# Kernel tuning notes

Hardware: AMD Instinct MI355X
Metric: run time of the kernel (lower is better)

Reference implementation:

```python
import jax, jax.numpy as jnp
import numpy as np

FP8_MAX = 448.0  # max finite value of float8_e4m3fn (the fwd fp8 dtype)


def fp8_quantize_dequantize(x):
    """Emulates load_ops_library.fp8_quantize followed by the dequant the
    fp8_matmul performs via its scale_inv tensors: per-tensor amax scaling,
    cast to e4m3 (round-to-nearest-even, saturating), cast back, unscale."""
    amax = jnp.max(jnp.abs(x))
    scale = FP8_MAX / jnp.maximum(amax, jnp.asarray(1e-12, x.dtype))
    q = (x * scale).astype(jnp.float8_e4m3fn).astype(x.dtype) / scale
    return q


def setup_inputs() -> dict:
    key = jax.random.key(0)
    k1, k2, k3 = jax.random.split(key, 3)
    tokens, d_in, units = 8192, 4096, 16384
    x = jax.random.normal(k1, (tokens, d_in), dtype=jnp.float32)
    # kernel ~ RandomNormal(mean=0, stddev=0.023) per the layer default
    kernel = 0.023 * jax.random.normal(k2, (d_in, units), dtype=jnp.float32)
    bias = 0.02 * jax.random.normal(k3, (units,), dtype=jnp.float32)
    return {"x": x, "kernel": kernel, "bias": bias}


def reference(x, kernel, bias):
    # fp8 path: quantize activations and kernel to e4m3, fp8 GEMM with fused
    # bias (emulated as dequantized f32 GEMM), then fused approximate gelu.
    xq = fp8_quantize_dequantize(x)          # [T, D] in e4m3 grid
    kq = fp8_quantize_dequantize(kernel)     # [D, U] in e4m3 grid
    out = jnp.dot(xq, kq) + bias             # [T, U]
    out = jax.nn.gelu(out, approximate=True) # tanh-approximate gelu
    return out
```

## Files before the change

kernel.cpp:

```cpp
#include <hip/hip_runtime.h>
#include <cstdint>
#include <cstddef>

namespace {

constexpr int T_DIM = 8192;
constexpr int D_DIM = 4096;
constexpr int U_DIM = 16384;

typedef float f32x4 __attribute__((ext_vector_type(4)));

__device__ __forceinline__ void gl_lds16(const void* g, void* l) {
  typedef const __attribute__((address_space(1))) unsigned int* gp_t;
  typedef __attribute__((address_space(3))) unsigned int* lp_t;
  __builtin_amdgcn_global_load_lds((gp_t)g, (lp_t)l, 16, 0, 0);
}

__global__ void amax_kernel(const float4* __restrict__ p, int n4,
                            unsigned* __restrict__ out) {
  float m = 0.f;
  const int stride = gridDim.x * blockDim.x;
  for (int i = blockIdx.x * blockDim.x + threadIdx.x; i < n4; i += stride) {
    float4 v = p[i];
    m = fmaxf(m, fmaxf(fmaxf(fabsf(v.x), fabsf(v.y)),
                       fmaxf(fabsf(v.z), fabsf(v.w))));
  }
#pragma unroll
  for (int off = 32; off > 0; off >>= 1)
    m = fmaxf(m, __shfl_down(m, off, 64));
  if ((threadIdx.x & 63) == 0) atomicMax(out, __float_as_uint(m));
}

__global__ void quant_x_kernel(const float4* __restrict__ x,
                               unsigned* __restrict__ xq, int n4,
                               const unsigned* __restrict__ amax_bits) {
  const float s = 448.f / fmaxf(__uint_as_float(amax_bits[0]), 1e-12f);
  const int stride = gridDim.x * blockDim.x;
  for (int i = blockIdx.x * blockDim.x + threadIdx.x; i < n4; i += stride) {
    float4 v = x[i];
    int pk = 0;
    pk = __builtin_amdgcn_cvt_pk_fp8_f32(v.x * s, v.y * s, pk, false);
    pk = __builtin_amdgcn_cvt_pk_fp8_f32(v.z * s, v.w * s, pk, true);
    xq[i] = (unsigned)pk;
  }
}

__global__ void quant_kT_kernel(const float* __restrict__ k,
                                unsigned char* __restrict__ kq,
                                const unsigned* __restrict__ amax_bits) {
  __shared__ float smf[64 * 65];
  const float s = 448.f / fmaxf(__uint_as_float(amax_bits[1]), 1e-12f);
  const int u0 = blockIdx.x * 64, d0 = blockIdx.y * 64;
  const int t = threadIdx.x;
  const int r0 = t >> 4, c4 = (t & 15) << 2;
#pragma unroll
  for (int rr = r0; rr < 64; rr += 16) {
    float4 v = *(const float4*)(k + (size_t)(d0 + rr) * U_DIM + u0 + c4);
    smf[(c4 + 0) * 65 + rr] = v.x;
    smf[(c4 + 1) * 65 + rr] = v.y;
    smf[(c4 + 2) * 65 + rr] = v.z;
    smf[(c4 + 3) * 65 + rr] = v.w;
  }
  __syncthreads();
#pragma unroll
  for (int rr = r0; rr < 64; rr += 16) {
    float a = smf[rr * 65 + c4 + 0];
    float b = smf[rr * 65 + c4 + 1];
    float c = smf[rr * 65 + c4 + 2];
    float d = smf[rr * 65 + c4 + 3];
    int pk = 0;
    pk = __builtin_amdgcn_cvt_pk_fp8_f32(a * s, b * s, pk, false);
    pk = __builtin_amdgcn_cvt_pk_fp8_f32(c * s, d * s, pk, true);
    *(unsigned*)(kq + (size_t)(u0 + rr) * D_DIM + d0 + c4) = (unsigned)pk;
  }
}


#define BAR() __builtin_amdgcn_s_barrier()
#define WLGKM() asm volatile("s_waitcnt lgkmcnt(0)" ::: "memory")
#define WVM_(N) asm volatile("s_waitcnt vmcnt(" #N ")" ::: "memory")
#define WVM(N) WVM_(N)
#define SBAR0() __builtin_amdgcn_sched_barrier(0)

#define LDA(MH)                                                         \
  do {                                                                  \
    _Pragma("unroll") for (int q2 = 0; q2 < 4; ++q2) {                  \
      _Pragma("unroll") for (int ks = 0; ks < 4; ++ks) {                \
        aR[q2][ks] = *(const long long*)&sh[aks[ks] +                   \
                                            ((MH)*64 + q2 * 16) * 128]; \
      }                                                                 \
    }                                                                   \
  } while (0)

#define LDB(NH)                                                       \
  do {                                                                \
    _Pragma("unroll") for (int j = 0; j < 2; ++j) {                   \
      _Pragma("unroll") for (int ks = 0; ks < 4; ++ks) {              \
        bR[j][ks] =                                                   \
            *(const long long*)&sh[bks[ks] + ((NH)*2 + j) * 2048];    \
      }                                                               \
    }                                                                 \
  } while (0)

#define MQ(MH, NH)                                                        \
  do {                                                                    \
    _Pragma("unroll") for (int ks = 0; ks < 4; ++ks) {                    \
      _Pragma("unroll") for (int q2 = 0; q2 < 4; ++q2) {                  \
        _Pragma("unroll") for (int j = 0; j < 2; ++j) {                   \
          acc[(MH)*4 + q2][(NH)*2 + j] =                                  \
              __builtin_amdgcn_mfma_f32_16x16x32_fp8_fp8(                 \
                  aR[q2][ks], bR[j][ks], acc[(MH)*4 + q2][(NH)*2 + j], 0, \
                  0, 0);                                                  \
        }                                                                 \
      }                                                                   \
    }                                                                     \
  } while (0)

#define STG_A(ROFF, LOFF, KB1) \
  gl_lds16(gA + (size_t)(ROFF)*D_DIM + (KB1), &sh[(LOFF) + ldst])
#define STG_B(ROFF, LOFF, KB1) \
  gl_lds16(gB + (size_t)(ROFF)*D_DIM + (KB1), &sh[65536 + (LOFF) + ldst])

#define TILE_BODY(ABUF, ANEXT, KB1, ST, VM1)                              \
  do {                                                                    \
    int aks[4], bks[4];                                                   \
    _Pragma("unroll") for (int ks = 0; ks < 4; ++ks) {                    \
      aks[ks] = ((ABUF) + arow) ^ (ks << 5);                              \
      bks[ks] = ((ABUF) + brow) ^ (ks << 5);                              \
    }                                                                     \
                              \
    LDA(0);                                                               \
    LDB(0);                                                               \
    if (ST) {                                                             \
      STG_B(0, (ANEXT) + 0, KB1);                                         \
      STG_B(128, (ANEXT) + 16384, KB1);                                   \
    }                                                                     \
    BAR();                                                                \
    WLGKM();                                                              \
    __builtin_amdgcn_s_setprio(1);                                        \
    MQ(0, 0);                                                             \
    __builtin_amdgcn_s_setprio(0);                                        \
    BAR();                                                                \
                                       \
    LDB(1);                                                               \
    if (ST) {                                                             \
      STG_B(64, (ANEXT) + 8192, KB1);                                     \
      STG_B(192, (ANEXT) + 24576, KB1);                                   \
    }                                                                     \
    BAR();                                                                \
    WLGKM();                                                              \
    __builtin_amdgcn_s_setprio(1);                                        \
    MQ(0, 1);                                                             \
    __builtin_amdgcn_s_setprio(0);                                        \
    WVM(VM1);                                                             \
    BAR();                                                                \
    SBAR0();        \
                                       \
    LDA(1);                                                               \
    LDB(0);                                                               \
    if (ST) {                                                             \
      STG_A(0, (ANEXT) + 0, KB1);                                         \
      STG_A(128, (ANEXT) + 16384, KB1);                                   \
    }                                                                     \
    BAR();                                                                \
    WLGKM();                                                              \
    __builtin_amdgcn_s_setprio(1);                                        \
    MQ(1, 0);                                                             \
    __builtin_amdgcn_s_setprio(0);                                        \
    BAR();                                                                \
                                       \
    LDB(1);                                                               \
    if (ST) {                                                             \
      STG_A(64, (ANEXT) + 8192, KB1);                                     \
      STG_A(192, (ANEXT) + 24576, KB1);                                   \
    }                                                                     \
    BAR();                                                                \
    WLGKM();                                                              \
    __builtin_amdgcn_s_setprio(1);                                        \
    MQ(1, 1);                                                             \
    __builtin_amdgcn_s_setprio(0);                                        \
    WVM(2);                                                               \
    BAR();                                                                \
    SBAR0();         \
  } while (0)

__global__ __launch_bounds__(512, 2) void gemm_fp8_kernel(
    const unsigned char* __restrict__ A, const unsigned char* __restrict__ B,
    const float* __restrict__ bias, const unsigned* __restrict__ amax_bits,
    float* __restrict__ out) {
  __shared__ __align__(128) unsigned char sh[131072];

  const int tid = threadIdx.x;
  const int lane = tid & 63;
  const int wave = tid >> 6;
  const int wr = wave >> 2, wc = wave & 3;
  const int lane15 = lane & 15;

  const int bid = (int)blockIdx.y * 64 + (int)blockIdx.x;
  const int swz = (bid & 7) * 256 + (bid >> 3);
  const size_t m0 = (size_t)(swz >> 6) * 256;
  const size_t n0 = (size_t)(swz & 63) * 256;

  const float sx = 448.f / fmaxf(__uint_as_float(amax_bits[0]), 1e-12f);
  const float sk = 448.f / fmaxf(__uint_as_float(amax_bits[1]), 1e-12f);
  const float inv_s = 1.f / (sx * sk);

  const int srow = tid >> 3;
  const int schunk = (((tid & 7) ^ (srow & 7)) << 4);
  const unsigned char* gA = A + (m0 + srow) * D_DIM + schunk;
  const unsigned char* gB = B + (n0 + srow) * D_DIM + schunk;
  const int ldst = tid * 16;

  const int kgs = (((lane >> 4) << 3) ^ ((lane & 7) << 4));
  const int arow = (wr * 128 + lane15) * 128 + kgs;
  const int brow = 65536 + (wc * 64 + lane15) * 128 + kgs;

  f32x4 acc[8][4];
#pragma unroll
  for (int i = 0; i < 8; ++i)
#pragma unroll
    for (int j = 0; j < 4; ++j) acc[i][j] = (f32x4){0.f, 0.f, 0.f, 0.f};
  long long aR[4][4];
  long long bR[2][4];

  STG_B(0, 0, 0);
  STG_B(128, 16384, 0);
  STG_B(64, 8192, 0);
  STG_B(192, 24576, 0);
  STG_A(0, 0, 0);
  STG_A(128, 16384, 0);
  STG_A(64, 8192, 0);
  STG_A(192, 24576, 0);
  asm volatile("s_waitcnt vmcnt(0)" ::: "memory");
  BAR();
  SBAR0();

  for (int tp = 0; tp < 15; ++tp) {
    const size_t kb1a = (size_t)(2 * tp + 1) * 128;
    const size_t kb1b = (size_t)(2 * tp + 2) * 128;
    TILE_BODY(0, 32768, kb1a, true, 4);
    TILE_BODY(32768, 0, kb1b, true, 4);
  }
  TILE_BODY(0, 32768, (size_t)31 * 128, true, 4);
  TILE_BODY(32768, 0, (size_t)0, false, 0);

  const int q4 = (lane >> 4) << 2;
  float bj[4];
#pragma unroll
  for (int j = 0; j < 4; ++j)
    bj[j] = bias[n0 + wc * 64 + j * 16 + lane15];

#pragma unroll
  for (int i = 0; i < 8; ++i) {
    const size_t grow_base = m0 + (size_t)(wr * 128 + i * 16 + q4);
#pragma unroll
    for (int r = 0; r < 4; ++r) {
      float* orow = out + (grow_base + r) * U_DIM + n0 + wc * 64 + lane15;
#pragma unroll
      for (int j = 0; j < 4; ++j) {
        float v = acc[i][j][r] * inv_s + bj[j];
        float uu = 0.7978845608028654f * (v + 0.044715f * v * v * v);
        float e = __expf(2.f * uu);
        float th = 1.f - 2.f / (e + 1.f);
        orow[j * 16] = 0.5f * v * (1.f + th);
      }
    }
  }
}

}

extern "C" void kernel_launch(void* const* d_in, const int* in_sizes, int n_in,
                              void* d_out, int out_size, void* d_ws,
                              size_t ws_size, hipStream_t stream) {
  const float* x = (const float*)d_in[0];
  const float* kern = (const float*)d_in[1];
  const float* bias = (const float*)d_in[2];
  float* out = (float*)d_out;

  unsigned char* ws = (unsigned char*)d_ws;
  unsigned* amax_bits = (unsigned*)ws;
  unsigned char* xq = ws + 256;
  unsigned char* kqt = ws + 256 + (size_t)T_DIM * D_DIM;

  hipMemsetAsync(d_ws, 0, 8, stream);

  amax_kernel<<<2048, 256, 0, stream>>>((const float4*)x, T_DIM * D_DIM / 4,
                                        amax_bits + 0);
  amax_kernel<<<4096, 256, 0, stream>>>((const float4*)kern, D_DIM * U_DIM / 4,
                                        amax_bits + 1);
  quant_x_kernel<<<2048, 256, 0, stream>>>((const float4*)x, (unsigned*)xq,
                                           T_DIM * D_DIM / 4, amax_bits);
  quant_kT_kernel<<<dim3(U_DIM / 64, D_DIM / 64), 256, 0, stream>>>(
      kern, kqt, amax_bits);
  gemm_fp8_kernel<<<dim3(U_DIM / 256, T_DIM / 256), 512, 0, stream>>>(
      xq, kqt, bias, amax_bits, out);
}
```

Baseline: 1.993 ms.

## Restructure GEMM tile loop into two phases with all-B register preload

Each k-tile is now split into two half-phases instead of four quarter-phases. The full B fragment set (4x4) is loaded into registers once per tile, and A fragments are loaded in small per-row-group chunks interleaved with their MFMAs. This removes several workgroup barriers and LDS waits per tile, lets LDS reads overlap with MFMA issue, and batches the global-to-LDS staging. The cost is that B now holds more registers while A holds fewer. Fewer barriers also give LDS latency less cover, and correctness depends on the vmcnt wait counts (4, 2) matching the batched stage issue.

```diff
diff --git a/kernel.cpp b/kernel.cpp
--- a/kernel.cpp
+++ b/kernel.cpp
@@ -82,36 +82,30 @@
 #define WVM(N) WVM_(N)
 #define SBAR0() __builtin_amdgcn_sched_barrier(0)
 
-#define LDA(MH)                                                         \
-  do {                                                                  \
-    _Pragma("unroll") for (int q2 = 0; q2 < 4; ++q2) {                  \
-      _Pragma("unroll") for (int ks = 0; ks < 4; ++ks) {                \
-        aR[q2][ks] = *(const long long*)&sh[aks[ks] +                   \
-                                            ((MH)*64 + q2 * 16) * 128]; \
-      }                                                                 \
-    }                                                                   \
-  } while (0)
-
-#define LDB(NH)                                                       \
-  do {                                                                \
-    _Pragma("unroll") for (int j = 0; j < 2; ++j) {                   \
-      _Pragma("unroll") for (int ks = 0; ks < 4; ++ks) {              \
-        bR[j][ks] =                                                   \
-            *(const long long*)&sh[bks[ks] + ((NH)*2 + j) * 2048];    \
-      }                                                               \
-    }                                                                 \
-  } while (0)
-
-#define MQ(MH, NH)                                                        \
+#define LDB_ALL()                                                   \
+  do {                                                              \
+    _Pragma("unroll") for (int jb = 0; jb < 4; ++jb) {              \
+      _Pragma("unroll") for (int ks = 0; ks < 4; ++ks) {            \
+        bR[jb][ks] = *(const long long*)&sh[bks[ks] + jb * 2048];   \
+      }                                                             \
+    }                                                               \
+  } while (0)
+
+#define LDA4(MH, Q2)                                                \
+  do {                                                              \
+    _Pragma("unroll") for (int ks = 0; ks < 4; ++ks) {              \
+      aR[ks] = *(const long long*)&sh[aks[ks] +                     \
+                                      ((MH)*64 + (Q2)*16) * 128];   \
+    }                                                               \
+  } while (0)
+
+#define MQ16(MH, Q2)                                                      \
   do {                                                                    \
     _Pragma("unroll") for (int ks = 0; ks < 4; ++ks) {                    \
-      _Pragma("unroll") for (int q2 = 0; q2 < 4; ++q2) {                  \
-        _Pragma("unroll") for (int j = 0; j < 2; ++j) {                   \
-          acc[(MH)*4 + q2][(NH)*2 + j] =                                  \
-              __builtin_amdgcn_mfma_f32_16x16x32_fp8_fp8(                 \
-                  aR[q2][ks], bR[j][ks], acc[(MH)*4 + q2][(NH)*2 + j], 0, \
-                  0, 0);                                                  \
-        }                                                                 \
+      _Pragma("unroll") for (int jb = 0; jb < 4; ++jb) {                  \
+        acc[(MH)*4 + (Q2)][jb] =                                          \
+            __builtin_amdgcn_mfma_f32_16x16x32_fp8_fp8(                   \
+                aR[ks], bR[jb][ks], acc[(MH)*4 + (Q2)][jb], 0, 0, 0);     \
       }                                                                   \
     }                                                                     \
   } while (0)
@@ -121,67 +115,48 @@
 #define STG_B(ROFF, LOFF, KB1) \
   gl_lds16(gB + (size_t)(ROFF)*D_DIM + (KB1), &sh[65536 + (LOFF) + ldst])
 
-#define TILE_BODY(ABUF, ANEXT, KB1, ST, VM1)                              \
+#define TILE2(ABUF, ANEXT, KB1, ST, VMP0, VMP1)                           \
   do {                                                                    \
     int aks[4], bks[4];                                                   \
     _Pragma("unroll") for (int ks = 0; ks < 4; ++ks) {                    \
       aks[ks] = ((ABUF) + arow) ^ (ks << 5);                              \
       bks[ks] = ((ABUF) + brow) ^ (ks << 5);                              \
     }                                                                     \
-                              \
-    LDA(0);                                                               \
-    LDB(0);                                                               \
+                                              \
+    LDB_ALL();                                                            \
     if (ST) {                                                             \
       STG_B(0, (ANEXT) + 0, KB1);                                         \
       STG_B(128, (ANEXT) + 16384, KB1);                                   \
-    }                                                                     \
-    BAR();                                                                \
-    WLGKM();                                                              \
-    __builtin_amdgcn_s_setprio(1);                                        \
-    MQ(0, 0);                                                             \
-    __builtin_amdgcn_s_setprio(0);                                        \
-    BAR();                                                                \
-                                       \
-    LDB(1);                                                               \
-    if (ST) {                                                             \
       STG_B(64, (ANEXT) + 8192, KB1);                                     \
       STG_B(192, (ANEXT) + 24576, KB1);                                   \
     }                                                                     \
     BAR();                                                                \
-    WLGKM();                                                              \
+    WLGKM();                                              \
     __builtin_amdgcn_s_setprio(1);                                        \
-    MQ(0, 1);                                                             \
+    _Pragma("unroll") for (int q2 = 0; q2 < 4; ++q2) {                    \
+      LDA4(0, q2);                                                        \
+      MQ16(0, q2);                                                        \
+    }                                                                     \
     __builtin_amdgcn_s_setprio(0);                                        \
-    WVM(VM1);                                                             \
+    WVM(VMP0);                                                            \
     BAR();                                                                \
     SBAR0();        \
-                                       \
-    LDA(1);                                                               \
-    LDB(0);                                                               \
+                                              \
     if (ST) {                                                             \
       STG_A(0, (ANEXT) + 0, KB1);                                         \
       STG_A(128, (ANEXT) + 16384, KB1);                                   \
-    }                                                                     \
-    BAR();                                                                \
-    WLGKM();                                                              \
-    __builtin_amdgcn_s_setprio(1);                                        \
-    MQ(1, 0);                                                             \
-    __builtin_amdgcn_s_setprio(0);                                        \
-    BAR();                                                                \
-                                       \
-    LDB(1);                                                               \
-    if (ST) {                                                             \
       STG_A(64, (ANEXT) + 8192, KB1);                                     \
       STG_A(192, (ANEXT) + 24576, KB1);                                   \
     }                                                                     \
+    __builtin_amdgcn_s_setprio(1);                                        \
+    _Pragma("unroll") for (int q2 = 0; q2 < 4; ++q2) {                    \
+      LDA4(1, q2);                                                        \
+      MQ16(1, q2);                                                        \
+    }                                                                     \
+    __builtin_amdgcn_s_setprio(0);                                        \
+    WVM(VMP1);                                                            \
     BAR();                                                                \
-    WLGKM();                                                              \
-    __builtin_amdgcn_s_setprio(1);                                        \
-    MQ(1, 1);                                                             \
-    __builtin_amdgcn_s_setprio(0);                                        \
-    WVM(2);                                                               \
-    BAR();                                                                \
-    SBAR0();         \
+    SBAR0();             \
   } while (0)
 
 __global__ __launch_bounds__(512, 2) void gemm_fp8_kernel(
@@ -220,8 +195,8 @@
   for (int i = 0; i < 8; ++i)
 #pragma unroll
     for (int j = 0; j < 4; ++j) acc[i][j] = (f32x4){0.f, 0.f, 0.f, 0.f};
-  long long aR[4][4];
-  long long bR[2][4];
+  long long aR[4];
+  long long bR[4][4];
 
   STG_B(0, 0, 0);
   STG_B(128, 16384, 0);
@@ -238,11 +213,11 @@
   for (int tp = 0; tp < 15; ++tp) {
     const size_t kb1a = (size_t)(2 * tp + 1) * 128;
     const size_t kb1b = (size_t)(2 * tp + 2) * 128;
-    TILE_BODY(0, 32768, kb1a, true, 4);
-    TILE_BODY(32768, 0, kb1b, true, 4);
-  }
-  TILE_BODY(0, 32768, (size_t)31 * 128, true, 4);
-  TILE_BODY(32768, 0, (size_t)0, false, 0);
+    TILE2(0, 32768, kb1a, true, 4, 2);
+    TILE2(32768, 0, kb1b, true, 4, 2);
+  }
+  TILE2(0, 32768, (size_t)31 * 128, true, 4, 2);
+  TILE2(32768, 0, (size_t)0, false, 0, 0);
 
   const int q4 = (lane >> 4) << 2;
   float bj[4];
```

Result: faster. 1.835 ms (-7.9%).
